# Kernel tuning notes

Hardware: AMD Instinct MI355X
Metric: run time of the kernel (lower is better)

Reference implementation:

```python
import jax, jax.numpy as jnp
import numpy as np

THRESHOLD = 1.0
WINDOW = 1.0 * THRESHOLD  # module-level `window = 1.0`, scaled by threshold at call site
THRESHOLD_LOW = -1.0
BATCH_SIZE = 32


@jax.custom_vjp
def threshold_subtract(v):
    # sinabs ThresholdSubtract forward: number of spikes = floor(v / threshold) for v > 0
    return jnp.where(v > 0, jnp.floor(v / THRESHOLD), jnp.zeros_like(v))

def _ts_fwd(v):
    return threshold_subtract(v), v

def _ts_bwd(v, g):
    # surrogate gradient: boxcar of width `window` below threshold, scaled by 1/threshold
    surrogate = (v >= (THRESHOLD - WINDOW)).astype(g.dtype) / THRESHOLD
    return (g * surrogate,)

threshold_subtract.defvjp(_ts_fwd, _ts_bwd)


def setup_inputs() -> dict:
    key = jax.random.key(0)
    # [time_steps * batch, features] = [64*32, 16384]; synaptic currents in [0, 1)
    binary_input = jax.random.uniform(key, (2048, 16384), dtype=jnp.float32)
    return {"binary_input": binary_input}


def reference(binary_input):
    # reshape to [T, B, F] as in forward() when batch_size is set
    syn_out = binary_input.reshape((-1, BATCH_SIZE) + binary_input.shape[1:])
    state0 = jnp.zeros(syn_out.shape[1:], dtype=syn_out.dtype)
    act0 = jnp.zeros_like(state0)

    def step(carry, x):
        state, activations = carry
        # membrane update with subtract-on-spike
        state = x + state - activations * THRESHOLD
        # lower-bound clamp: relu(state - threshold_low) + threshold_low
        state = jax.nn.relu(state - THRESHOLD_LOW) + THRESHOLD_LOW
        activations = threshold_subtract(state)
        return (state, activations), activations

    _, all_spikes = jax.lax.scan(step, (state0, act0), syn_out)  # [T, B, F]
    # reshape back to [T*B, F]
    return all_spikes.reshape((-1,) + all_spikes.shape[2:])
```

## Files before the change

### kernel.cpp

```cpp
#include <hip/hip_runtime.h>


#define T_STEPS 64
#define NCHAINS (32 * 16384)
#define NCHAINS4 (NCHAINS / 4)

__device__ __forceinline__ void step1(float x, float& s, float& a) {
    s = (x + s) - a;
    s = fmaxf(s + 1.0f, 0.0f) - 1.0f;
    a = (s > 0.0f) ? floorf(s) : 0.0f;
}

__global__ __launch_bounds__(256) void spiking_kernel(
    const float4* __restrict__ in, float4* __restrict__ out) {
    const int i = blockIdx.x * blockDim.x + threadIdx.x;

    float4 s = {0.f, 0.f, 0.f, 0.f};
    float4 a = {0.f, 0.f, 0.f, 0.f};

    float4 x0 = in[i];
    float4 x1 = in[NCHAINS4 + i];

    for (int t = 0; t < T_STEPS; ++t) {
        float4 x = x0;
        x0 = x1;
        int tn = t + 2 < T_STEPS ? t + 2 : T_STEPS - 1;
        x1 = in[tn * NCHAINS4 + i];

        step1(x.x, s.x, a.x);
        step1(x.y, s.y, a.y);
        step1(x.z, s.z, a.z);
        step1(x.w, s.w, a.w);

        out[t * NCHAINS4 + i] = a;
    }
}

extern "C" void kernel_launch(void* const* d_in, const int* in_sizes, int n_in,
                              void* d_out, int out_size, void* d_ws, size_t ws_size,
                              hipStream_t stream) {
    const float4* in = (const float4*)d_in[0];
    float4* out = (float4*)d_out;
    spiking_kernel<<<NCHAINS4 / 256, 256, 0, stream>>>(in, out);
}
```

Before: 221.2 us.

## Use one chain per thread with scalar loads and 8-deep register prefetch

Switches from float4-per-thread processing to one scalar chain per thread, quadrupling the thread count. It also replaces the 2-deep prefetch with a fully unrolled 8-deep register prefetch ring. The aim is more outstanding memory requests to hide DRAM latency in this streaming recurrence. The trade-off is narrower per-instruction memory accesses and more threads to schedule.

```diff
diff --git a/kernel.cpp b/kernel.cpp
--- a/kernel.cpp
+++ b/kernel.cpp
@@ -3,43 +3,35 @@
 
 #define T_STEPS 64
 #define NCHAINS (32 * 16384)
-#define NCHAINS4 (NCHAINS / 4)
+#define PF 8
 
-__device__ __forceinline__ void step1(float x, float& s, float& a) {
-    s = (x + s) - a;
-    s = fmaxf(s + 1.0f, 0.0f) - 1.0f;
-    a = (s > 0.0f) ? floorf(s) : 0.0f;
-}
-
-__global__ __launch_bounds__(256) void spiking_kernel(
-    const float4* __restrict__ in, float4* __restrict__ out) {
+__global__ __launch_bounds__(256, 8) void spiking_kernel(
+    const float* __restrict__ in, float* __restrict__ out) {
     const int i = blockIdx.x * blockDim.x + threadIdx.x;
 
-    float4 s = {0.f, 0.f, 0.f, 0.f};
-    float4 a = {0.f, 0.f, 0.f, 0.f};
+    float s = 0.f, a = 0.f;
+    float xs[PF];
 
-    float4 x0 = in[i];
-    float4 x1 = in[NCHAINS4 + i];
+    #pragma unroll
+    for (int j = 0; j < PF; ++j) xs[j] = in[j * NCHAINS + i];
 
+    #pragma unroll
     for (int t = 0; t < T_STEPS; ++t) {
-        float4 x = x0;
-        x0 = x1;
-        int tn = t + 2 < T_STEPS ? t + 2 : T_STEPS - 1;
-        x1 = in[tn * NCHAINS4 + i];
+        float x = xs[t % PF];
+        if (t + PF < T_STEPS) xs[t % PF] = in[(t + PF) * NCHAINS + i];
 
-        step1(x.x, s.x, a.x);
-        step1(x.y, s.y, a.y);
-        step1(x.z, s.z, a.z);
-        step1(x.w, s.w, a.w);
+        s = (x + s) - a;
+        s = fmaxf(s + 1.0f, 0.0f) - 1.0f;
+        a = (s > 0.0f) ? floorf(s) : 0.0f;
 
-        out[t * NCHAINS4 + i] = a;
+        out[t * NCHAINS + i] = a;
     }
 }
 
 extern "C" void kernel_launch(void* const* d_in, const int* in_sizes, int n_in,
                               void* d_out, int out_size, void* d_ws, size_t ws_size,
                               hipStream_t stream) {
-    const float4* in = (const float4*)d_in[0];
-    float4* out = (float4*)d_out;
-    spiking_kernel<<<NCHAINS4 / 256, 256, 0, stream>>>(in, out);
+    const float* in = (const float*)d_in[0];
+    float* out = (float*)d_out;
+    spiking_kernel<<<NCHAINS / 256, 256, 0, stream>>>(in, out);
 }
```

Result: slower. 231.4 us (+4.6%).
